# Kernel tuning notes

Measured on AMD Instinct MI355X. Metric: run time of the kernel, lower is better.

The kernel has to match this reference:

```python
import jax, jax.numpy as jnp
import numpy as np

B, D, T = 16, 512, 2048
K, C = 8, 1024          # num_codebooks, codebook_size
CH = D // K             # chunk_size = 64
COMMIT = 0.25
EPS = 1e-8


def setup_inputs() -> dict:
    key = jax.random.key(0)
    k1, k2 = jax.random.split(key)
    x = jax.random.normal(k1, (B, D, T), dtype=jnp.float32)
    # kaiming-uniform-ish init for codebooks [K, C, CH]
    bound = float(np.sqrt(6.0 / CH))
    codebooks = jax.random.uniform(k2, (K, C, CH), dtype=jnp.float32,
                                   minval=-bound, maxval=bound)
    return {"x": x, "codebooks": codebooks}


def reference(x, codebooks):
    b, d, t = x.shape
    xc = x.reshape(b, K, CH, t)                       # [B,K,CH,T]
    x_norm = jnp.sum(xc * xc, axis=2)[:, :, None, :]  # [B,K,1,T]
    c_norm = jnp.sum(codebooks * codebooks, axis=2)[None, :, :, None]  # [1,K,C,1]
    cross = -2.0 * jnp.einsum('bkdt,kcd->bkct', xc, codebooks)         # [B,K,C,T]
    distances = x_norm + c_norm + cross
    indices = jnp.argmin(distances, axis=2)           # [B,K,T] int
    # gather nearest codewords -> [B,K,T,CH] -> [B,K,CH,T]
    q = codebooks[jnp.arange(K)[None, :, None], indices]
    q = jnp.transpose(q, (0, 1, 3, 2))                # [B,K,CH,T]
    # per-codebook usage histogram
    kk = jnp.broadcast_to(jnp.arange(K)[None, :, None], indices.shape)
    counts = jnp.zeros((K, C), dtype=jnp.float32).at[kk.ravel(), indices.ravel()].add(1.0)
    avg_probs = counts / (b * t)
    perplexity = jnp.exp(jnp.sum(-avg_probs * jnp.log(avg_probs + EPS), axis=1))
    # commitment losses
    sg = jax.lax.stop_gradient
    codebook_loss = jnp.mean((sg(xc) - q) ** 2)
    encoder_loss = jnp.mean((xc - sg(q)) ** 2)
    commit_loss = codebook_loss + COMMIT * encoder_loss
    # straight-through estimator
    quantized = xc + sg(q - xc)
    return quantized.reshape(b, d, t), commit_loss, perplexity
```

## Files before the change

kernel.cpp:

```cpp
#include <hip/hip_runtime.h>
#include <hip/hip_bf16.h>
#include <math.h>

#define B_   16
#define D_   512
#define T_   2048
#define K_   8
#define C_   1024
#define CH_  64
#define NEL_ (B_ * D_ * T_)
#define QOFF 16777216

#define WS_HCN   0
#define WS_CNT   32768
#define WS_SSE   65536
#define WS_CBS   66048

typedef __attribute__((ext_vector_type(8))) short   short8;
typedef __attribute__((ext_vector_type(8))) __bf16  bf16x8;
typedef __attribute__((ext_vector_type(4))) float   f32x4;

__device__ __forceinline__ unsigned short f2bf_rne(float f) {
    unsigned u = __builtin_bit_cast(unsigned, f);
    u = u + 0x7FFFu + ((u >> 16) & 1u);
    return (unsigned short)(u >> 16);
}

__device__ __forceinline__ void gload_lds16(const void* gsrc, void* ldst) {
    __builtin_amdgcn_global_load_lds(
        (const __attribute__((address_space(1))) unsigned int*)gsrc,
        (__attribute__((address_space(3))) unsigned int*)ldst,
        16, 0, 0);
}

__global__ void vq_prep(const float* __restrict__ cb,
                        unsigned char* __restrict__ cbS,
                        float* __restrict__ hcn) {
    int g   = blockIdx.x * 256 + threadIdx.x;
    int row = g >> 3;
    int s8  = g & 7;
    const float* src = cb + (size_t)row * CH_;

    short8 val;
#pragma unroll
    for (int j = 0; j < 8; ++j)
        val[j] = (short)f2bf_rne(-src[s8 * 8 + j]);
    *(short8*)(cbS + (size_t)row * 128 + ((s8 ^ (row & 7)) * 16)) = val;

    if (s8 == 0) {
        float s = 0.f;
#pragma unroll 8
        for (int ch = 0; ch < CH_; ++ch) {
            float v = src[ch];
            s = fmaf(v, v, s);
        }
        hcn[row] = 0.5f * s;
    }
}

#define LDSBUF 16384

__global__ __launch_bounds__(256) void vq_main(
    const float* __restrict__ x,
    const float* __restrict__ cb,
    const unsigned char* __restrict__ cbS,
    const float* __restrict__ hcn,
    float* __restrict__ out,
    int* __restrict__ counts,
    double* __restrict__ sse)
{
    __shared__ __align__(16) unsigned char lds[2 * LDSBUF + 4096];
    float* hcnS = (float*)(lds + 2 * LDSBUF);

    const int tid  = threadIdx.x;
    const int lane = tid & 63;
    const int wave = tid >> 6;
    const int ln   = lane & 15;
    const int q    = lane >> 4;
    const int q4   = q * 4;

    const int bid = blockIdx.x;
    const int tc  = bid & 15;
    const int k   = (bid >> 4) & 7;
    const int b   = bid >> 7;
    const int t0  = tc * 128 + wave * 32;

    short8 bh[2][2];
    for (int tt = 0; tt < 2; ++tt) {
        int t = t0 + tt * 16 + ln;
        for (int ks = 0; ks < 2; ++ks) {
            const float* xp = x + ((size_t)(b * D_ + k * CH_ + ks * 32 + q * 8)) * T_ + t;
            short8 sh;
#pragma unroll
            for (int j = 0; j < 8; ++j)
                sh[j] = (short)f2bf_rne(xp[(size_t)j * T_]);
            bh[tt][ks] = sh;
        }
    }

    const unsigned char* cbS_k = cbS + (size_t)k * C_ * 128;
    const float*         hcn_k = hcn + k * C_;

    for (int i = tid; i < C_; i += 256) hcnS[i] = hcn_k[i];

    {
        const unsigned char* src = cbS_k + wave * 4096 + lane * 16;
        unsigned char* dst = lds + wave * 4096;
#pragma unroll
        for (int i = 0; i < 4; ++i)
            gload_lds16(src + i * 1024, dst + i * 1024);
    }

    float md[2][4];
    int   mj[2][4];
#pragma unroll
    for (int tt = 0; tt < 2; ++tt)
#pragma unroll
        for (int r = 0; r < 4; ++r) { md[tt][r] = INFINITY; mj[tt][r] = 0; }

    for (int chunk = 0; chunk < 8; ++chunk) {
        __syncthreads();

        if (chunk < 7) {
            const unsigned char* src =
                cbS_k + (size_t)(chunk + 1) * 16384 + wave * 4096 + lane * 16;
            unsigned char* dst = lds + ((chunk + 1) & 1) * LDSBUF + wave * 4096;
#pragma unroll
            for (int i = 0; i < 4; ++i)
                gload_lds16(src + i * 1024, dst + i * 1024);
        }

        const unsigned char* buf = lds + (chunk & 1) * LDSBUF;
#pragma unroll
        for (int sub = 0; sub < 8; ++sub) {
            const unsigned char* rowb = buf + (sub * 16 + ln) * 128;
            f32x4 h4 = *(const f32x4*)(hcnS + chunk * 128 + sub * 16 + q4);
            f32x4 a0 = h4, a1 = h4;
#pragma unroll
            for (int ks = 0; ks < 2; ++ks) {
                int cidx = ((ks * 4 + q) ^ (ln & 7)) * 16;
                bf16x8 ah = __builtin_bit_cast(bf16x8, *(const short8*)(rowb + cidx));
                a0 = __builtin_amdgcn_mfma_f32_16x16x32_bf16(ah, __builtin_bit_cast(bf16x8, bh[0][ks]), a0, 0, 0, 0);
                a1 = __builtin_amdgcn_mfma_f32_16x16x32_bf16(ah, __builtin_bit_cast(bf16x8, bh[1][ks]), a1, 0, 0, 0);
            }
            const int j = chunk * 8 + sub;
#pragma unroll
            for (int r = 0; r < 4; ++r) {
                bool lt0 = a0[r] < md[0][r];
                md[0][r] = lt0 ? a0[r] : md[0][r];
                mj[0][r] = lt0 ? j : mj[0][r];
                bool lt1 = a1[r] < md[1][r];
                md[1][r] = lt1 ? a1[r] : md[1][r];
                mj[1][r] = lt1 ? j : mj[1][r];
            }
        }
    }

    double waveSse = 0.0;
    const float* cb_k = cb + (size_t)k * C_ * CH_;

    for (int tt = 0; tt < 2; ++tt) {
        const int t = t0 + tt * 16 + ln;

        float d1 = md[tt][0], d2 = INFINITY;
        int   c1 = mj[tt][0] * 16 + q * 4, c2 = 0;
#pragma unroll
        for (int r = 1; r < 4; ++r) {
            float v  = md[tt][r];
            int   cv = mj[tt][r] * 16 + q * 4 + r;
            bool b1 = v < d1;
            bool b2 = v < d2;
            float nd2 = b1 ? d1 : (b2 ? v : d2);
            int   nc2 = b1 ? c1 : (b2 ? cv : c2);
            d1 = b1 ? v : d1;
            c1 = b1 ? cv : c1;
            d2 = nd2; c2 = nc2;
        }
#pragma unroll
        for (int off = 16; off <= 32; off <<= 1) {
            float od1 = __shfl_xor(d1, off);
            int   oc1 = __shfl_xor(c1, off);
            float od2 = __shfl_xor(d2, off);
            int   oc2 = __shfl_xor(c2, off);
            if (od1 < d1) {
                float nd2 = (d1 < od2) ? d1 : od2;
                int   nc2 = (d1 < od2) ? c1 : oc2;
                d1 = od1; c1 = oc1; d2 = nd2; c2 = nc2;
            } else {
                float nd2 = (od1 < d2) ? od1 : d2;
                int   nc2 = (od1 < d2) ? oc1 : c2;
                d2 = nd2; c2 = nc2;
            }
        }

        const int half = q & 1;
        const int cc   = (lane >= 32) ? c2 : c1;
        const float* crow = cb_k + (size_t)cc * CH_ + half * 32;
        const float* xcol = x + ((size_t)(b * D_ + k * CH_ + half * 32)) * T_ + t;
        double s = 0.0;
#pragma unroll
        for (int ch = 0; ch < 32; ++ch) {
            double e = (double)xcol[(size_t)ch * T_] - (double)crow[ch];
            s = fma(e, e, s);
        }
        s += __shfl_xor(s, 16);
        double so = __shfl_xor(s, 32);
        double s1 = (lane < 32) ? s : so;
        double s2 = (lane < 32) ? so : s;
        bool pick2 = (s2 < s1) || (s2 == s1 && c2 < c1);
        int    idx = pick2 ? c2 : c1;
        double dm  = pick2 ? s2 : s1;

        if (q == 0) {
            waveSse += dm;
            atomicAdd(&counts[k * C_ + idx], 1);
        }

        const float* qrow = cb_k + (size_t)idx * CH_ + q * 16;
        float* op = out + ((size_t)(b * D_ + k * CH_ + q * 16)) * T_ + t;
#pragma unroll
        for (int jj = 0; jj < 4; ++jj) {
            float4 qv = *(const float4*)(qrow + 4 * jj);
            op[(size_t)(4 * jj + 0) * T_] = qv.x;
            op[(size_t)(4 * jj + 1) * T_] = qv.y;
            op[(size_t)(4 * jj + 2) * T_] = qv.z;
            op[(size_t)(4 * jj + 3) * T_] = qv.w;
        }
    }

    for (int off = 32; off > 0; off >>= 1) waveSse += __shfl_down(waveSse, off);
    if (lane == 0) atomicAdd(sse, waveSse);
}

__global__ void vq_final(const int* __restrict__ counts,
                         const double* __restrict__ sse,
                         float* __restrict__ out) {
    __shared__ double part[4];
    const int tid = threadIdx.x;
    const int k   = blockIdx.x;
    double local = 0.0;
    for (int j = tid; j < C_; j += 256) {
        double p = (double)counts[k * C_ + j] * (1.0 / (double)(B_ * T_));
        local += -p * log(p + 1e-8);
    }
    for (int off = 32; off > 0; off >>= 1) local += __shfl_down(local, off);
    if ((tid & 63) == 0) part[tid >> 6] = local;
    __syncthreads();
    if (tid == 0) {
        double sum = part[0] + part[1] + part[2] + part[3];
        out[QOFF + 1 + k] = (float)exp(sum);
        if (k == 0)
            out[QOFF] = (float)(1.25 * (*sse) / (double)NEL_);
    }
}

extern "C" void kernel_launch(void* const* d_in, const int* in_sizes, int n_in,
                              void* d_out, int out_size, void* d_ws, size_t ws_size,
                              hipStream_t stream) {
    const float* x  = (const float*)d_in[0];
    const float* cb = (const float*)d_in[1];
    float* out = (float*)d_out;

    float*         hcn    = (float*)((char*)d_ws + WS_HCN);
    int*           counts = (int*)((char*)d_ws + WS_CNT);
    double*        sse    = (double*)((char*)d_ws + WS_SSE);
    unsigned char* cbS    = (unsigned char*)((char*)d_ws + WS_CBS);

    hipMemsetAsync((char*)d_ws + WS_CNT, 0, 33024, stream);

    vq_prep<<<(K_ * C_ * 8) / 256, 256, 0, stream>>>(cb, cbS, hcn);
    vq_main<<<B_ * K_ * (T_ / 128), 256, 0, stream>>>(x, cb, cbS, hcn,
                                                      out, counts, sse);
    vq_final<<<K_, 256, 0, stream>>>(counts, sse, out);
}
```

Measured before the change: 237.0 us.

## Widen per-wave T tile to 64 and drop fp64 top-2 rescoring

Each wave now handles 64 time positions (4 MFMA tiles), so every codebook fragment read from LDS feeds four MFMAs instead of two, and the grid is halved. The exact fp64 re-evaluation of the top-2 candidates is removed. The argmin now uses the bf16 MFMA distance directly, with index tie-breaking. The SSE is rebuilt from the precomputed x norm plus twice the approximate distance. This cuts the strided global re-reads and fp64 math in the epilogue, at the cost of more registers (launch bounds now ask for 4 blocks). Index choice may differ from the fp32 reference on near ties, and the loss picks up bf16 error.

```diff
diff --git a/kernel.cpp b/kernel.cpp
--- a/kernel.cpp
+++ b/kernel.cpp
@@ -60,7 +60,7 @@
 
 #define LDSBUF 16384
 
-__global__ __launch_bounds__(256) void vq_main(
+__global__ __launch_bounds__(256, 4) void vq_main(
     const float* __restrict__ x,
     const float* __restrict__ cb,
     const unsigned char* __restrict__ cbS,
@@ -80,22 +80,32 @@
     const int q4   = q * 4;
 
     const int bid = blockIdx.x;
-    const int tc  = bid & 15;
-    const int k   = (bid >> 4) & 7;
-    const int b   = bid >> 7;
-    const int t0  = tc * 128 + wave * 32;
-
-    short8 bh[2][2];
-    for (int tt = 0; tt < 2; ++tt) {
+    const int tc  = bid & 7;
+    const int k   = (bid >> 3) & 7;
+    const int b   = bid >> 6;
+    const int t0  = tc * 256 + wave * 64;
+
+    short8 bh[4][2];
+    float  xn[4];
+#pragma unroll
+    for (int tt = 0; tt < 4; ++tt) {
         int t = t0 + tt * 16 + ln;
+        float pn = 0.f;
+#pragma unroll
         for (int ks = 0; ks < 2; ++ks) {
             const float* xp = x + ((size_t)(b * D_ + k * CH_ + ks * 32 + q * 8)) * T_ + t;
             short8 sh;
 #pragma unroll
-            for (int j = 0; j < 8; ++j)
-                sh[j] = (short)f2bf_rne(xp[(size_t)j * T_]);
+            for (int j = 0; j < 8; ++j) {
+                float v = xp[(size_t)j * T_];
+                pn = fmaf(v, v, pn);
+                sh[j] = (short)f2bf_rne(v);
+            }
             bh[tt][ks] = sh;
         }
+        pn += __shfl_xor(pn, 16);
+        pn += __shfl_xor(pn, 32);
+        xn[tt] = pn;
     }
 
     const unsigned char* cbS_k = cbS + (size_t)k * C_ * 128;
@@ -111,10 +121,10 @@
             gload_lds16(src + i * 1024, dst + i * 1024);
     }
 
-    float md[2][4];
-    int   mj[2][4];
-#pragma unroll
-    for (int tt = 0; tt < 2; ++tt)
+    float md[4][4];
+    int   mj[4][4];
+#pragma unroll
+    for (int tt = 0; tt < 4; ++tt)
 #pragma unroll
         for (int r = 0; r < 4; ++r) { md[tt][r] = INFINITY; mj[tt][r] = 0; }
 
@@ -135,23 +145,27 @@
         for (int sub = 0; sub < 8; ++sub) {
             const unsigned char* rowb = buf + (sub * 16 + ln) * 128;
             f32x4 h4 = *(const f32x4*)(hcnS + chunk * 128 + sub * 16 + q4);
-            f32x4 a0 = h4, a1 = h4;
+            f32x4 a[4];
+#pragma unroll
+            for (int tt = 0; tt < 4; ++tt) a[tt] = h4;
 #pragma unroll
             for (int ks = 0; ks < 2; ++ks) {
                 int cidx = ((ks * 4 + q) ^ (ln & 7)) * 16;
                 bf16x8 ah = __builtin_bit_cast(bf16x8, *(const short8*)(rowb + cidx));
-                a0 = __builtin_amdgcn_mfma_f32_16x16x32_bf16(ah, __builtin_bit_cast(bf16x8, bh[0][ks]), a0, 0, 0, 0);
-                a1 = __builtin_amdgcn_mfma_f32_16x16x32_bf16(ah, __builtin_bit_cast(bf16x8, bh[1][ks]), a1, 0, 0, 0);
+#pragma unroll
+                for (int tt = 0; tt < 4; ++tt)
+                    a[tt] = __builtin_amdgcn_mfma_f32_16x16x32_bf16(
+                        ah, __builtin_bit_cast(bf16x8, bh[tt][ks]), a[tt], 0, 0, 0);
             }
             const int j = chunk * 8 + sub;
 #pragma unroll
-            for (int r = 0; r < 4; ++r) {
-                bool lt0 = a0[r] < md[0][r];
-                md[0][r] = lt0 ? a0[r] : md[0][r];
-                mj[0][r] = lt0 ? j : mj[0][r];
-                bool lt1 = a1[r] < md[1][r];
-                md[1][r] = lt1 ? a1[r] : md[1][r];
-                mj[1][r] = lt1 ? j : mj[1][r];
+            for (int tt = 0; tt < 4; ++tt) {
+#pragma unroll
+                for (int r = 0; r < 4; ++r) {
+                    bool lt = a[tt][r] < md[tt][r];
+                    md[tt][r] = lt ? a[tt][r] : md[tt][r];
+                    mj[tt][r] = lt ? j : mj[tt][r];
+                }
             }
         }
     }
@@ -159,60 +173,32 @@
     double waveSse = 0.0;
     const float* cb_k = cb + (size_t)k * C_ * CH_;
 
-    for (int tt = 0; tt < 2; ++tt) {
+#pragma unroll
+    for (int tt = 0; tt < 4; ++tt) {
         const int t = t0 + tt * 16 + ln;
 
-        float d1 = md[tt][0], d2 = INFINITY;
-        int   c1 = mj[tt][0] * 16 + q * 4, c2 = 0;
+        float d1 = md[tt][0];
+        int   c1 = mj[tt][0] * 16 + q4;
 #pragma unroll
         for (int r = 1; r < 4; ++r) {
             float v  = md[tt][r];
-            int   cv = mj[tt][r] * 16 + q * 4 + r;
-            bool b1 = v < d1;
-            bool b2 = v < d2;
-            float nd2 = b1 ? d1 : (b2 ? v : d2);
-            int   nc2 = b1 ? c1 : (b2 ? cv : c2);
-            d1 = b1 ? v : d1;
-            c1 = b1 ? cv : c1;
-            d2 = nd2; c2 = nc2;
+            int   cv = mj[tt][r] * 16 + q4 + r;
+            bool w = (v < d1) || (v == d1 && cv < c1);
+            d1 = w ? v : d1;
+            c1 = w ? cv : c1;
         }
 #pragma unroll
         for (int off = 16; off <= 32; off <<= 1) {
-            float od1 = __shfl_xor(d1, off);
-            int   oc1 = __shfl_xor(c1, off);
-            float od2 = __shfl_xor(d2, off);
-            int   oc2 = __shfl_xor(c2, off);
-            if (od1 < d1) {
-                float nd2 = (d1 < od2) ? d1 : od2;
-                int   nc2 = (d1 < od2) ? c1 : oc2;
-                d1 = od1; c1 = oc1; d2 = nd2; c2 = nc2;
-            } else {
-                float nd2 = (od1 < d2) ? od1 : d2;
-                int   nc2 = (od1 < d2) ? oc1 : c2;
-                d2 = nd2; c2 = nc2;
-            }
-        }
-
-        const int half = q & 1;
-        const int cc   = (lane >= 32) ? c2 : c1;
-        const float* crow = cb_k + (size_t)cc * CH_ + half * 32;
-        const float* xcol = x + ((size_t)(b * D_ + k * CH_ + half * 32)) * T_ + t;
-        double s = 0.0;
-#pragma unroll
-        for (int ch = 0; ch < 32; ++ch) {
-            double e = (double)xcol[(size_t)ch * T_] - (double)crow[ch];
-            s = fma(e, e, s);
-        }
-        s += __shfl_xor(s, 16);
-        double so = __shfl_xor(s, 32);
-        double s1 = (lane < 32) ? s : so;
-        double s2 = (lane < 32) ? so : s;
-        bool pick2 = (s2 < s1) || (s2 == s1 && c2 < c1);
-        int    idx = pick2 ? c2 : c1;
-        double dm  = pick2 ? s2 : s1;
+            float ov = __shfl_xor(d1, off);
+            int   oc = __shfl_xor(c1, off);
+            bool w = (ov < d1) || (ov == d1 && oc < c1);
+            d1 = w ? ov : d1;
+            c1 = w ? oc : c1;
+        }
+        const int idx = c1;
 
         if (q == 0) {
-            waveSse += dm;
+            waveSse += (double)(xn[tt] + 2.0f * d1);
             atomicAdd(&counts[k * C_ + idx], 1);
         }
 
@@ -269,7 +255,7 @@
     hipMemsetAsync((char*)d_ws + WS_CNT, 0, 33024, stream);
 
     vq_prep<<<(K_ * C_ * 8) / 256, 256, 0, stream>>>(cb, cbS, hcn);
-    vq_main<<<B_ * K_ * (T_ / 128), 256, 0, stream>>>(x, cb, cbS, hcn,
+    vq_main<<<B_ * K_ * (T_ / 256), 256, 0, stream>>>(x, cb, cbS, hcn,
                                                       out, counts, sse);
     vq_final<<<K_, 256, 0, stream>>>(counts, sse, out);
 }
```

New measurement: 222.0 us. 1.07x faster.
